# Optimization experiments

Measured on AMD Instinct MI355X. Metric: run time of the kernel, lower is better.

The kernel has to match this reference:

```python
import jax, jax.numpy as jnp
import numpy as np
from jax import lax

N_INPUT, N_HIDDEN, N_OUTPUT = 1024, 2048, 1024
T, B = 512, 64

def setup_inputs() -> dict:
    key = jax.random.key(0)
    k_x, k_ih, k_hh, k_out = jax.random.split(key, 4)
    stdv = 1.0 / np.sqrt(N_HIDDEN)
    xs = jax.random.normal(k_x, (T, B, N_INPUT), dtype=jnp.float32)
    # torch nn.Linear weights are [out_features, in_features], init U(-stdv, stdv)
    W_ih = jax.random.uniform(k_ih, (N_HIDDEN, N_INPUT), jnp.float32, -stdv, stdv)
    W_hh = jax.random.uniform(k_hh, (N_HIDDEN, N_HIDDEN), jnp.float32, -stdv, stdv)
    W_out = jax.random.uniform(k_out, (N_OUTPUT, N_HIDDEN), jnp.float32, -stdv, stdv)
    return {"xs": xs, "W_ih": W_ih, "W_hh": W_hh, "W_out": W_out}

def reference(xs, W_ih, W_hh, W_out):
    # xs: [T, B, n_input] time-major. state starts as None -> relu(W_ih x),
    # which equals relu(W_ih x + W_hh * 0), so h0 = zeros is exact.
    n_hidden = W_hh.shape[0]
    h0 = jnp.zeros((xs.shape[1], n_hidden), dtype=xs.dtype)

    def step(h, x):
        h = jax.nn.relu(x @ W_ih.T + h @ W_hh.T)  # [B, n_hidden]
        return h, h

    _, h_seq = lax.scan(step, h0, xs)        # [T, B, n_hidden]
    ys = h_seq @ W_out.T                     # [T, B, n_output]
    return jnp.transpose(ys, (1, 0, 2))      # [B, T, n_output] (transpose(0,1))
```

## Files before the change

### kernel.cpp

```cpp
#include <hip/hip_runtime.h>
#include <hip/hip_bf16.h>
#include <stdint.h>


#define TT 512
#define BB 64
#define NIN 1024
#define NH 2048
#define NOUT 1024

typedef __attribute__((ext_vector_type(8))) short bf8;
typedef __attribute__((ext_vector_type(4))) float f4;
typedef __attribute__((ext_vector_type(4))) unsigned int u4;

static __device__ __forceinline__ unsigned short f2bf(float f) {
  __hip_bfloat16 h = __float2bfloat16(f);
  return __builtin_bit_cast(unsigned short, h);
}
static __device__ __forceinline__ float bf2f(unsigned short v) {
  return __bfloat162float(__builtin_bit_cast(__hip_bfloat16, v));
}
static __device__ __forceinline__ u4 pack8(const float* f) {
  u4 r;
#pragma unroll
  for (int i = 0; i < 4; ++i) {
    unsigned lo = f2bf(f[2 * i]);
    unsigned hi = f2bf(f[2 * i + 1]);
    r[i] = lo | (hi << 16);
  }
  return r;
}

static __device__ __forceinline__ size_t sl_idx(int m, int col) {
  return ((((size_t)(m >> 6) * 4 + ((m & 63) >> 4)) * 64 + (col >> 5)) << 9) +
         (size_t)((m & 63) & 15) * 32 + (col & 31);
}

template <bool ABF, bool TRANS>
__global__ void gemm_bt(const void* __restrict__ Av, const float* __restrict__ Bw,
                        void* __restrict__ Cv, unsigned char* __restrict__ plane,
                        int M, int N, int K) {
  constexpr int BM = 128, BN = 128, BK = 32;
  __shared__ u4 As[BM * 4];
  __shared__ u4 Bs[BN * 4];
  const int nt = N / BN;
  const int mi = (int)blockIdx.x / nt;
  const int ni = (int)blockIdx.x % nt;
  const int m0 = mi * BM, n0 = ni * BN;
  const int t = threadIdx.x;
  const int l = t & 63, w = t >> 6, wr = w >> 1, wc = w & 1;
  const int lr = l & 15, lq = l >> 4;

  f4 acc[4][4] = {};

  const int srow = t >> 1;
  const int sc0 = (t & 1) * 2;
  const u4 msk = {0x7fff7fffu, 0x7fff7fffu, 0x7fff7fffu, 0x7fff7fffu};

  for (int kt = 0; kt < K; kt += BK) {
    if (ABF) {
      const unsigned short* A = (const unsigned short*)Av;
#pragma unroll
      for (int cc = 0; cc < 2; ++cc) {
        int c = sc0 + cc;
        u4 v = *(const u4*)(A + sl_idx(m0 + srow, kt + c * 8));
        v &= msk;
        As[srow * 4 + (c ^ ((srow ^ (srow >> 2)) & 3))] = v;
      }
    } else {
      const float* A = (const float*)Av;
#pragma unroll
      for (int cc = 0; cc < 2; ++cc) {
        int c = sc0 + cc;
        const float* p = A + (size_t)(m0 + srow) * K + kt + c * 8;
        float4 v0 = *(const float4*)p;
        float4 v1 = *(const float4*)(p + 4);
        float f[8] = {v0.x, v0.y, v0.z, v0.w, v1.x, v1.y, v1.z, v1.w};
        As[srow * 4 + (c ^ ((srow ^ (srow >> 2)) & 3))] = pack8(f);
      }
    }
#pragma unroll
    for (int cc = 0; cc < 2; ++cc) {
      int c = sc0 + cc;
      const float* p = Bw + (size_t)(n0 + srow) * K + kt + c * 8;
      float4 v0 = *(const float4*)p;
      float4 v1 = *(const float4*)(p + 4);
      float f[8] = {v0.x, v0.y, v0.z, v0.w, v1.x, v1.y, v1.z, v1.w};
      Bs[srow * 4 + (c ^ ((srow ^ (srow >> 2)) & 3))] = pack8(f);
    }
    __syncthreads();

    bf8 a[4], b[4];
#pragma unroll
    for (int i = 0; i < 4; ++i) {
      int ra = wr * 64 + i * 16 + lr;
      a[i] = __builtin_bit_cast(bf8, As[ra * 4 + (lq ^ ((ra ^ (ra >> 2)) & 3))]);
      int rb = wc * 64 + i * 16 + lr;
      b[i] = __builtin_bit_cast(bf8, Bs[rb * 4 + (lq ^ ((rb ^ (rb >> 2)) & 3))]);
    }
#pragma unroll
    for (int i = 0; i < 4; ++i)
#pragma unroll
      for (int j = 0; j < 4; ++j)
        acc[i][j] = __builtin_amdgcn_mfma_f32_16x16x32_bf16(a[i], b[j], acc[i][j], 0, 0, 0);
    __syncthreads();
  }

  if (TRANS) {
    float* C = (float*)Cv;
#pragma unroll
    for (int i = 0; i < 4; ++i)
#pragma unroll
      for (int j = 0; j < 4; ++j)
#pragma unroll
        for (int r = 0; r < 4; ++r) {
          int m = m0 + wr * 64 + i * 16 + lq * 4 + r;
          int n = n0 + wc * 64 + j * 16 + lr;
          C[(size_t)(m & 63) * (TT * NOUT) + (size_t)(m >> 6) * NOUT + n] = acc[i][j][r];
        }
  } else {
    unsigned short* C = (unsigned short*)Cv;
#pragma unroll
    for (int i = 0; i < 4; ++i)
#pragma unroll
      for (int j = 0; j < 4; ++j)
#pragma unroll
        for (int r = 0; r < 4; ++r) {
          int m = m0 + wr * 64 + i * 16 + lq * 4 + r;
          int n = n0 + wc * 64 + j * 16 + lr;
          unsigned short v = f2bf(acc[i][j][r]);
          size_t sl = sl_idx(m, n);
          C[sl] = (unsigned short)(v & 0x7fffu);
          unsigned long long bal = __ballot((v & 0x8000u) != 0);
          if ((l & 7) == 0)
            plane[sl >> 3] = (unsigned char)((bal >> (l & ~7)) & 0xffull);
        }
  }
}

__global__ __launch_bounds__(512, 2) void rnn_recur(unsigned short* __restrict__ hseq,
                                                    const unsigned char* __restrict__ plane,
                                                    const float* __restrict__ Whh,
                                                    unsigned* __restrict__ flags) {
  __shared__ u4 Wl[32 * 256];
  __shared__ float red[2][4][16][36];
  const int t = threadIdx.x;
  const int bid = (int)blockIdx.x;
  const int g = (bid & 7) >> 1;
  const int jb = ((bid >> 3) << 1) | (bid & 1);
  const int j0 = jb * 32;

  {
    const int jl = t >> 4;
    const int ci = t & 15;
#pragma unroll
    for (int q = 0; q < 16; ++q) {
      int cc = ci * 16 + q;
      const float* p = Whh + (size_t)(j0 + jl) * NH + cc * 8;
      float4 v0 = *(const float4*)p;
      float4 v1 = *(const float4*)(p + 4);
      float f[8] = {v0.x, v0.y, v0.z, v0.w, v1.x, v1.y, v1.z, v1.w};
      Wl[jl * 256 + (cc ^ (jl & 7))] = pack8(f);
    }
  }

  const int l = t & 63, w = t >> 6;
  const int lr = l & 15, lq = l >> 4;
  const int kg = w >> 1, jh = w & 1;

  char* hb = (char*)hseq;
  const size_t gofs = (size_t)g << 16;
  const u4 msk = {0x7fff7fffu, 0x7fff7fffu, 0x7fff7fffu, 0x7fff7fffu};

  const int wr_r = l >> 2;
  const int wjq = l & 3;
  const size_t wbyte = (size_t)wr_r * 64 + jh * 32 + wjq * 8;

  unsigned long long pre = 0;
  unsigned nib = 0;

  __syncthreads();

  if (w < 2) {
    size_t e0 = gofs + ((size_t)jb << 10) + wbyte;
    unsigned long long p0 = __hip_atomic_load((const unsigned long long*)(hb + e0),
                                              __ATOMIC_RELAXED, __HIP_MEMORY_SCOPE_AGENT);
    unsigned nib0 = (plane[e0 >> 4] >> (((e0 >> 3) & 1) * 4)) & 0xfu;
    unsigned long long hv = 0x8000800080008000ull;
#pragma unroll
    for (int i = 0; i < 4; ++i)
      if (!((nib0 >> i) & 1u)) hv |= ((p0 >> (16 * i)) & 0x7fffull) << (16 * i);
    __hip_atomic_store((unsigned long long*)(hb + e0), hv, __ATOMIC_RELAXED,
                       __HIP_MEMORY_SCOPE_AGENT);
    if (l == 0)
      __hip_atomic_store(flags + ((g * 64 + jb) * 2 + w), 1u, __ATOMIC_RELAXED,
                         __HIP_MEMORY_SCOPE_AGENT);
    size_t e1 = ((size_t)4 << 16) + gofs + ((size_t)jb << 10) + wbyte;
    pre = __hip_atomic_load((const unsigned long long*)(hb + e1), __ATOMIC_RELAXED,
                            __HIP_MEMORY_SCOPE_AGENT);
    nib = (plane[e1 >> 4] >> (((e1 >> 3) & 1) * 4)) & 0xfu;
  }

  for (int ts = 1; ts < TT; ++ts) {
    {
      const unsigned* fp = flags + ((g * 64 + kg * 16 + (l >> 1)) * 2 + (l & 1));
      long spins = 0;
      for (;;) {
        unsigned fv = (l < 32) ? __hip_atomic_load(fp, __ATOMIC_RELAXED,
                                                   __HIP_MEMORY_SCOPE_AGENT)
                               : 0xffffffffu;
        if (__ballot(fv >= (unsigned)ts) == ~0ull) break;
        __builtin_amdgcn_s_sleep(1);
        if (++spins > (1L << 22)) break;
      }
    }
    asm volatile("" ::: "memory");

    const size_t rowoff = (size_t)(l & 15) * 64 + (size_t)(l >> 4) * 16;
    const size_t base =
        (((size_t)(ts - 1) * 4) << 16) + gofs + ((size_t)(kg * 16) << 10) + rowoff;
    unsigned long long a0 = (unsigned long long)(uintptr_t)(hb + base);
    unsigned long long a1 = a0 + 4096;
    unsigned long long a2 = a0 + 8192;
    unsigned long long a3 = a0 + 12288;
    u4 av[16];
    int att = 0;
    for (;;) {
      asm volatile(
          "global_load_dwordx4 %0, %16, off sc0 sc1\n\t"
          "global_load_dwordx4 %1, %16, off offset:1024 sc0 sc1\n\t"
          "global_load_dwordx4 %2, %16, off offset:2048 sc0 sc1\n\t"
          "global_load_dwordx4 %3, %16, off offset:3072 sc0 sc1\n\t"
          "global_load_dwordx4 %4, %17, off sc0 sc1\n\t"
          "global_load_dwordx4 %5, %17, off offset:1024 sc0 sc1\n\t"
          "global_load_dwordx4 %6, %17, off offset:2048 sc0 sc1\n\t"
          "global_load_dwordx4 %7, %17, off offset:3072 sc0 sc1\n\t"
          "global_load_dwordx4 %8, %18, off sc0 sc1\n\t"
          "global_load_dwordx4 %9, %18, off offset:1024 sc0 sc1\n\t"
          "global_load_dwordx4 %10, %18, off offset:2048 sc0 sc1\n\t"
          "global_load_dwordx4 %11, %18, off offset:3072 sc0 sc1\n\t"
          "global_load_dwordx4 %12, %19, off sc0 sc1\n\t"
          "global_load_dwordx4 %13, %19, off offset:1024 sc0 sc1\n\t"
          "global_load_dwordx4 %14, %19, off offset:2048 sc0 sc1\n\t"
          "global_load_dwordx4 %15, %19, off offset:3072 sc0 sc1\n\t"
          "s_waitcnt vmcnt(0)"
          : "=&v"(av[0]), "=&v"(av[1]), "=&v"(av[2]), "=&v"(av[3]),
            "=&v"(av[4]), "=&v"(av[5]), "=&v"(av[6]), "=&v"(av[7]),
            "=&v"(av[8]), "=&v"(av[9]), "=&v"(av[10]), "=&v"(av[11]),
            "=&v"(av[12]), "=&v"(av[13]), "=&v"(av[14]), "=&v"(av[15])
          : "v"(a0), "v"(a1), "v"(a2), "v"(a3)
          : "memory");
      unsigned am = 0xffffffffu;
#pragma unroll
      for (int c = 0; c < 16; ++c)
#pragma unroll
        for (int d = 0; d < 4; ++d) am &= av[c][d];
      bool ok = (am & 0x80008000u) == 0x80008000u;
      if (__ballot(ok) == ~0ull) break;
      __builtin_amdgcn_s_sleep(1);
      if (++att > (1 << 20)) break;
    }

    f4 acc0 = {}, acc1 = {};
#pragma unroll
    for (int c = 0; c < 16; ++c) {
      u4 v = av[c] & msk;
      bf8 af = __builtin_bit_cast(bf8, v);
      int ci = kg * 64 + c * 4 + lq;
      bf8 bfr = __builtin_bit_cast(bf8, Wl[(jh * 16 + lr) * 256 + (ci ^ (lr & 7))]);
      if (c & 1)
        acc1 = __builtin_amdgcn_mfma_f32_16x16x32_bf16(af, bfr, acc1, 0, 0, 0);
      else
        acc0 = __builtin_amdgcn_mfma_f32_16x16x32_bf16(af, bfr, acc0, 0, 0, 0);
    }
    f4 a2v = acc0 + acc1;

    const int buf = ts & 1;
#pragma unroll
    for (int i = 0; i < 4; ++i) red[buf][kg][(l >> 4) * 4 + i][jh * 16 + (l & 15)] = a2v[i];
    __syncthreads();

    if (w < 2) {
      __builtin_amdgcn_s_setprio(1);
      float pf[4];
#pragma unroll
      for (int i = 0; i < 4; ++i) {
        unsigned pv = (unsigned)((pre >> (16 * i)) & 0xffffull);
        pv |= ((nib >> i) & 1u) << 15;
        pf[i] = bf2f((unsigned short)pv);
      }
      f4 s = {};
#pragma unroll
      for (int q = 0; q < 4; ++q) s += *(const f4*)&red[buf][q][wr_r][jh * 16 + wjq * 4];
      unsigned long long hv = 0;
#pragma unroll
      for (int i = 0; i < 4; ++i) {
        float v = s[i] + pf[i];
        v = v > 0.f ? v : 0.f;
        hv |= (unsigned long long)(unsigned short)(f2bf(v) | 0x8000u) << (16 * i);
      }
      size_t eo = (((size_t)ts * 4) << 16) + gofs + ((size_t)jb << 10) + wbyte;
      __hip_atomic_store((unsigned long long*)(hb + eo), hv, __ATOMIC_RELAXED,
                         __HIP_MEMORY_SCOPE_AGENT);
      if (l == 0)
        __hip_atomic_store(flags + ((g * 64 + jb) * 2 + w), (unsigned)(ts + 1),
                           __ATOMIC_RELAXED, __HIP_MEMORY_SCOPE_AGENT);
      if (ts + 1 < TT) {
        size_t en = (((size_t)(ts + 1) * 4) << 16) + gofs + ((size_t)jb << 10) + wbyte;
        pre = __hip_atomic_load((const unsigned long long*)(hb + en), __ATOMIC_RELAXED,
                                __HIP_MEMORY_SCOPE_AGENT);
        nib = (plane[en >> 4] >> (((en >> 3) & 1) * 4)) & 0xfu;
      }
      __builtin_amdgcn_s_setprio(0);
    }
  }
}

__global__ void kinit(unsigned* f) { f[threadIdx.x] = 0u; }

extern "C" void kernel_launch(void* const* d_in, const int* in_sizes, int n_in,
                              void* d_out, int out_size, void* d_ws, size_t ws_size,
                              hipStream_t stream) {
  const float* xs = (const float*)d_in[0];
  const float* Wih = (const float*)d_in[1];
  const float* Whh = (const float*)d_in[2];
  const float* Wout = (const float*)d_in[3];

  unsigned short* hseq = (unsigned short*)d_ws;
  unsigned char* plane = (unsigned char*)d_ws + ((size_t)TT * BB * NH * 2);
  unsigned* flags = (unsigned*)(plane + ((size_t)TT * BB * NH / 8));

  kinit<<<1, 512, 0, stream>>>(flags);

  gemm_bt<false, false><<<(TT * BB / 128) * (NH / 128), 256, 0, stream>>>(
      (const void*)xs, Wih, (void*)hseq, plane, TT * BB, NH, NIN);

  rnn_recur<<<256, 512, 0, stream>>>(hseq, plane, Whh, flags);

  gemm_bt<true, true><<<(TT * BB / 128) * (NOUT / 128), 256, 0, stream>>>(
      (const void*)hseq, Wout, d_out, plane, TT * BB, NOUT, NH);
}
```

Baseline: 3.848 ms.

## Repartition recurrence into 8 batch groups with register-resident W_hh slices

The recurrent kernel now splits the batch into 8 groups of 8 rows and the hidden dimension into 32 blocks of 64 columns, in place of 4 groups of 16 rows and 64 blocks of 32 columns. Each wave keeps its W_hh slice in registers instead of LDS. Each step cooperatively loads the previous hidden state once per block into LDS, with one contiguous 64-byte load per thread, instead of each wave doing 16 strided polling loads. The hidden-state slab layout changes to 8-row by 64-column tiles to match, and the upstream GEMM is updated to read and write that layout. The aim is fewer global polling loads and fewer flags to wait on per step. In exchange there is an extra barrier per step, higher register pressure from the weights, and half of each MFMA's rows are unused because only 8 batch rows are valid.

```diff
diff --git a/kernel.cpp b/kernel.cpp
--- a/kernel.cpp
+++ b/kernel.cpp
@@ -31,9 +31,9 @@
   return r;
 }
 
-static __device__ __forceinline__ size_t sl_idx(int m, int col) {
-  return ((((size_t)(m >> 6) * 4 + ((m & 63) >> 4)) * 64 + (col >> 5)) << 9) +
-         (size_t)((m & 63) & 15) * 32 + (col & 31);
+static __device__ __forceinline__ size_t sl_idx8(int m, int col) {
+  return ((((size_t)(m >> 6) * 8 + ((m & 63) >> 3)) * 32 + (col >> 6)) << 9) +
+         (size_t)((m & 63) & 7) * 64 + (col & 63);
 }
 
 template <bool ABF, bool TRANS>
@@ -63,7 +63,7 @@
 #pragma unroll
       for (int cc = 0; cc < 2; ++cc) {
         int c = sc0 + cc;
-        u4 v = *(const u4*)(A + sl_idx(m0 + srow, kt + c * 8));
+        u4 v = *(const u4*)(A + sl_idx8(m0 + srow, kt + c * 8));
         v &= msk;
         As[srow * 4 + (c ^ ((srow ^ (srow >> 2)) & 3))] = v;
       }
@@ -129,7 +129,7 @@
           int m = m0 + wr * 64 + i * 16 + lq * 4 + r;
           int n = n0 + wc * 64 + j * 16 + lr;
           unsigned short v = f2bf(acc[i][j][r]);
-          size_t sl = sl_idx(m, n);
+          size_t sl = sl_idx8(m, n);
           C[sl] = (unsigned short)(v & 0x7fffu);
           unsigned long long bal = __ballot((v & 0x8000u) != 0);
           if ((l & 7) == 0)
@@ -142,47 +142,45 @@
                                                     const unsigned char* __restrict__ plane,
                                                     const float* __restrict__ Whh,
                                                     unsigned* __restrict__ flags) {
-  __shared__ u4 Wl[32 * 256];
-  __shared__ float red[2][4][16][36];
+  __shared__ u4 hs[8 * 256];
+  __shared__ float red[2][4][8][68];
   const int t = threadIdx.x;
   const int bid = (int)blockIdx.x;
-  const int g = (bid & 7) >> 1;
-  const int jb = ((bid >> 3) << 1) | (bid & 1);
-  const int j0 = jb * 32;
-
-  {
-    const int jl = t >> 4;
-    const int ci = t & 15;
-#pragma unroll
-    for (int q = 0; q < 16; ++q) {
-      int cc = ci * 16 + q;
-      const float* p = Whh + (size_t)(j0 + jl) * NH + cc * 8;
+  const int g = bid & 7;
+  const int jb = bid >> 3;
+  const int j0 = jb * 64;
+
+  const int l = t & 63, w = t >> 6;
+  const int lr = l & 15, lq = l >> 4;
+  const int kg = w >> 1, jh = w & 1;
+
+  u4 wreg[2][16];
+#pragma unroll
+  for (int jt = 0; jt < 2; ++jt) {
+    const float* p0 = Whh + (size_t)(j0 + jh * 32 + jt * 16 + lr) * NH + kg * 512 + lq * 8;
+#pragma unroll
+    for (int ks = 0; ks < 16; ++ks) {
+      const float* p = p0 + ks * 32;
       float4 v0 = *(const float4*)p;
       float4 v1 = *(const float4*)(p + 4);
       float f[8] = {v0.x, v0.y, v0.z, v0.w, v1.x, v1.y, v1.z, v1.w};
-      Wl[jl * 256 + (cc ^ (jl & 7))] = pack8(f);
-    }
-  }
-
-  const int l = t & 63, w = t >> 6;
-  const int lr = l & 15, lq = l >> 4;
-  const int kg = w >> 1, jh = w & 1;
+      wreg[jt][ks] = pack8(f);
+    }
+  }
 
   char* hb = (char*)hseq;
-  const size_t gofs = (size_t)g << 16;
   const u4 msk = {0x7fff7fffu, 0x7fff7fffu, 0x7fff7fffu, 0x7fff7fffu};
 
-  const int wr_r = l >> 2;
-  const int wjq = l & 3;
-  const size_t wbyte = (size_t)wr_r * 64 + jh * 32 + wjq * 8;
+  const size_t wbyte = (size_t)(l >> 3) * 128 + (size_t)jh * 64 + (size_t)(l & 7) * 8;
+  const int sr = (t & 15) >> 1;
+  const int scb = ((t >> 4) << 3) + (t & 1) * 4;
+  const int fidx = (g * 32 + (t >> 4)) * 2 + (t & 1);
 
   unsigned long long pre = 0;
   unsigned nib = 0;
 
-  __syncthreads();
-
   if (w < 2) {
-    size_t e0 = gofs + ((size_t)jb << 10) + wbyte;
+    size_t e0 = (((size_t)g * 32 + jb) << 10) + wbyte;
     unsigned long long p0 = __hip_atomic_load((const unsigned long long*)(hb + e0),
                                               __ATOMIC_RELAXED, __HIP_MEMORY_SCOPE_AGENT);
     unsigned nib0 = (plane[e0 >> 4] >> (((e0 >> 3) & 1) * 4)) & 0xfu;
@@ -193,9 +191,9 @@
     __hip_atomic_store((unsigned long long*)(hb + e0), hv, __ATOMIC_RELAXED,
                        __HIP_MEMORY_SCOPE_AGENT);
     if (l == 0)
-      __hip_atomic_store(flags + ((g * 64 + jb) * 2 + w), 1u, __ATOMIC_RELAXED,
+      __hip_atomic_store(flags + ((g * 32 + jb) * 2 + w), 1u, __ATOMIC_RELAXED,
                          __HIP_MEMORY_SCOPE_AGENT);
-    size_t e1 = ((size_t)4 << 16) + gofs + ((size_t)jb << 10) + wbyte;
+    size_t e1 = (((size_t)(1 * 8 + g) * 32 + jb) << 10) + wbyte;
     pre = __hip_atomic_load((const unsigned long long*)(hb + e1), __ATOMIC_RELAXED,
                             __HIP_MEMORY_SCOPE_AGENT);
     nib = (plane[e1 >> 4] >> (((e1 >> 3) & 1) * 4)) & 0xfu;
@@ -203,12 +201,10 @@
 
   for (int ts = 1; ts < TT; ++ts) {
     {
-      const unsigned* fp = flags + ((g * 64 + kg * 16 + (l >> 1)) * 2 + (l & 1));
+      const unsigned* fp = flags + fidx;
       long spins = 0;
       for (;;) {
-        unsigned fv = (l < 32) ? __hip_atomic_load(fp, __ATOMIC_RELAXED,
-                                                   __HIP_MEMORY_SCOPE_AGENT)
-                               : 0xffffffffu;
+        unsigned fv = __hip_atomic_load(fp, __ATOMIC_RELAXED, __HIP_MEMORY_SCOPE_AGENT);
         if (__ballot(fv >= (unsigned)ts) == ~0ull) break;
         __builtin_amdgcn_s_sleep(1);
         if (++spins > (1L << 22)) break;
@@ -216,68 +212,63 @@
     }
     asm volatile("" ::: "memory");
 
-    const size_t rowoff = (size_t)(l & 15) * 64 + (size_t)(l >> 4) * 16;
-    const size_t base =
-        (((size_t)(ts - 1) * 4) << 16) + gofs + ((size_t)(kg * 16) << 10) + rowoff;
-    unsigned long long a0 = (unsigned long long)(uintptr_t)(hb + base);
-    unsigned long long a1 = a0 + 4096;
-    unsigned long long a2 = a0 + 8192;
-    unsigned long long a3 = a0 + 12288;
-    u4 av[16];
-    int att = 0;
-    for (;;) {
-      asm volatile(
-          "global_load_dwordx4 %0, %16, off sc0 sc1\n\t"
-          "global_load_dwordx4 %1, %16, off offset:1024 sc0 sc1\n\t"
-          "global_load_dwordx4 %2, %16, off offset:2048 sc0 sc1\n\t"
-          "global_load_dwordx4 %3, %16, off offset:3072 sc0 sc1\n\t"
-          "global_load_dwordx4 %4, %17, off sc0 sc1\n\t"
-          "global_load_dwordx4 %5, %17, off offset:1024 sc0 sc1\n\t"
-          "global_load_dwordx4 %6, %17, off offset:2048 sc0 sc1\n\t"
-          "global_load_dwordx4 %7, %17, off offset:3072 sc0 sc1\n\t"
-          "global_load_dwordx4 %8, %18, off sc0 sc1\n\t"
-          "global_load_dwordx4 %9, %18, off offset:1024 sc0 sc1\n\t"
-          "global_load_dwordx4 %10, %18, off offset:2048 sc0 sc1\n\t"
-          "global_load_dwordx4 %11, %18, off offset:3072 sc0 sc1\n\t"
-          "global_load_dwordx4 %12, %19, off sc0 sc1\n\t"
-          "global_load_dwordx4 %13, %19, off offset:1024 sc0 sc1\n\t"
-          "global_load_dwordx4 %14, %19, off offset:2048 sc0 sc1\n\t"
-          "global_load_dwordx4 %15, %19, off offset:3072 sc0 sc1\n\t"
-          "s_waitcnt vmcnt(0)"
-          : "=&v"(av[0]), "=&v"(av[1]), "=&v"(av[2]), "=&v"(av[3]),
-            "=&v"(av[4]), "=&v"(av[5]), "=&v"(av[6]), "=&v"(av[7]),
-            "=&v"(av[8]), "=&v"(av[9]), "=&v"(av[10]), "=&v"(av[11]),
-            "=&v"(av[12]), "=&v"(av[13]), "=&v"(av[14]), "=&v"(av[15])
-          : "v"(a0), "v"(a1), "v"(a2), "v"(a3)
-          : "memory");
-      unsigned am = 0xffffffffu;
-#pragma unroll
-      for (int c = 0; c < 16; ++c)
-#pragma unroll
-        for (int d = 0; d < 4; ++d) am &= av[c][d];
-      bool ok = (am & 0x80008000u) == 0x80008000u;
-      if (__ballot(ok) == ~0ull) break;
-      __builtin_amdgcn_s_sleep(1);
-      if (++att > (1 << 20)) break;
-    }
-
-    f4 acc0 = {}, acc1 = {};
-#pragma unroll
-    for (int c = 0; c < 16; ++c) {
-      u4 v = av[c] & msk;
-      bf8 af = __builtin_bit_cast(bf8, v);
-      int ci = kg * 64 + c * 4 + lq;
-      bf8 bfr = __builtin_bit_cast(bf8, Wl[(jh * 16 + lr) * 256 + (ci ^ (lr & 7))]);
-      if (c & 1)
-        acc1 = __builtin_amdgcn_mfma_f32_16x16x32_bf16(af, bfr, acc1, 0, 0, 0);
-      else
-        acc0 = __builtin_amdgcn_mfma_f32_16x16x32_bf16(af, bfr, acc0, 0, 0, 0);
-    }
-    f4 a2v = acc0 + acc1;
+    const size_t goff = ((((size_t)(ts - 1) * 8 + g) * 32) << 10) + (size_t)t * 64;
+    unsigned long long ga = (unsigned long long)(uintptr_t)(hb + goff);
+    u4 av[4];
+    {
+      long att = 0;
+      for (;;) {
+        asm volatile(
+            "global_load_dwordx4 %0, %4, off sc0 sc1\n\t"
+            "global_load_dwordx4 %1, %4, off offset:16 sc0 sc1\n\t"
+            "global_load_dwordx4 %2, %4, off offset:32 sc0 sc1\n\t"
+            "global_load_dwordx4 %3, %4, off offset:48 sc0 sc1\n\t"
+            "s_waitcnt vmcnt(0)"
+            : "=&v"(av[0]), "=&v"(av[1]), "=&v"(av[2]), "=&v"(av[3])
+            : "v"(ga)
+            : "memory");
+        unsigned am = 0xffffffffu;
+#pragma unroll
+        for (int c = 0; c < 4; ++c)
+#pragma unroll
+          for (int d = 0; d < 4; ++d) am &= av[c][d];
+        bool ok = (am & 0x80008000u) == 0x80008000u;
+        if (__ballot(ok) == ~0ull) break;
+        __builtin_amdgcn_s_sleep(1);
+        if (++att > (1L << 20)) break;
+      }
+    }
+#pragma unroll
+    for (int ch = 0; ch < 4; ++ch)
+      hs[sr * 256 + ((scb + ch) ^ sr)] = av[ch] & msk;
+    __syncthreads();
+
+    const int arow = l & 7;
+    f4 aA0 = {}, aA1 = {}, aB0 = {}, aB1 = {};
+#pragma unroll
+    for (int ks = 0; ks < 16; ++ks) {
+      u4 a = hs[arow * 256 + ((kg * 64 + ks * 4 + lq) ^ arow)];
+      bf8 af = __builtin_bit_cast(bf8, a);
+      bf8 b0 = __builtin_bit_cast(bf8, wreg[0][ks]);
+      bf8 b1 = __builtin_bit_cast(bf8, wreg[1][ks]);
+      if (ks & 1) {
+        aA1 = __builtin_amdgcn_mfma_f32_16x16x32_bf16(af, b0, aA1, 0, 0, 0);
+        aB1 = __builtin_amdgcn_mfma_f32_16x16x32_bf16(af, b1, aB1, 0, 0, 0);
+      } else {
+        aA0 = __builtin_amdgcn_mfma_f32_16x16x32_bf16(af, b0, aA0, 0, 0, 0);
+        aB0 = __builtin_amdgcn_mfma_f32_16x16x32_bf16(af, b1, aB0, 0, 0, 0);
+      }
+    }
+    f4 aA = aA0 + aA1, aB = aB0 + aB1;
 
     const int buf = ts & 1;
-#pragma unroll
-    for (int i = 0; i < 4; ++i) red[buf][kg][(l >> 4) * 4 + i][jh * 16 + (l & 15)] = a2v[i];
+    if (lq < 2) {
+#pragma unroll
+      for (int i = 0; i < 4; ++i) {
+        red[buf][kg][lq * 4 + i][jh * 32 + lr] = aA[i];
+        red[buf][kg][lq * 4 + i][jh * 32 + 16 + lr] = aB[i];
+      }
+    }
     __syncthreads();
 
     if (w < 2) {
@@ -289,9 +280,11 @@
         pv |= ((nib >> i) & 1u) << 15;
         pf[i] = bf2f((unsigned short)pv);
       }
+      const int rr = l >> 3;
+      const int jq = l & 7;
       f4 s = {};
 #pragma unroll
-      for (int q = 0; q < 4; ++q) s += *(const f4*)&red[buf][q][wr_r][jh * 16 + wjq * 4];
+      for (int q = 0; q < 4; ++q) s += *(const f4*)&red[buf][q][rr][jh * 32 + jq * 4];
       unsigned long long hv = 0;
 #pragma unroll
       for (int i = 0; i < 4; ++i) {
@@ -299,14 +292,14 @@
         v = v > 0.f ? v : 0.f;
         hv |= (unsigned long long)(unsigned short)(f2bf(v) | 0x8000u) << (16 * i);
       }
-      size_t eo = (((size_t)ts * 4) << 16) + gofs + ((size_t)jb << 10) + wbyte;
+      size_t eo = (((size_t)ts * 8 + g) * 32 + jb) * 1024 + wbyte;
       __hip_atomic_store((unsigned long long*)(hb + eo), hv, __ATOMIC_RELAXED,
                          __HIP_MEMORY_SCOPE_AGENT);
       if (l == 0)
-        __hip_atomic_store(flags + ((g * 64 + jb) * 2 + w), (unsigned)(ts + 1),
+        __hip_atomic_store(flags + ((g * 32 + jb) * 2 + w), (unsigned)(ts + 1),
                            __ATOMIC_RELAXED, __HIP_MEMORY_SCOPE_AGENT);
       if (ts + 1 < TT) {
-        size_t en = (((size_t)(ts + 1) * 4) << 16) + gofs + ((size_t)jb << 10) + wbyte;
+        size_t en = (((size_t)(ts + 1) * 8 + g) * 32 + jb) * 1024 + wbyte;
         pre = __hip_atomic_load((const unsigned long long*)(hb + en), __ATOMIC_RELAXED,
                                 __HIP_MEMORY_SCOPE_AGENT);
         nib = (plane[en >> 4] >> (((en >> 3) & 1) * 4)) & 0xfu;
```

Result: slower. 5.024 ms (+30.6%).

## Overlap hidden-state loads with MFMA via staged waitcnt and per-chunk readiness retry

Applied to the files above, without the earlier changes.

The recurrent step used to issue all 16 hidden-state loads, wait for every one, check readiness flags across the whole tile, and retry the whole set if any chunk was stale. Now the loads complete in four groups using partial vmcnt waits, and each 16-byte chunk gets its own readiness check and its MFMA as soon as that group arrives. Only chunks that fail the check are reloaded individually afterwards. The aim is to overlap memory latency with matrix math and avoid reloading the full tile on a partial miss. In exchange it adds per-chunk ballots and branches and relies on inline-asm waitcnt ordering being correct.

```diff
diff --git a/kernel.cpp b/kernel.cpp
--- a/kernel.cpp
+++ b/kernel.cpp
@@ -224,54 +224,95 @@
     unsigned long long a2 = a0 + 8192;
     unsigned long long a3 = a0 + 12288;
     u4 av[16];
-    int att = 0;
-    for (;;) {
-      asm volatile(
-          "global_load_dwordx4 %0, %16, off sc0 sc1\n\t"
-          "global_load_dwordx4 %1, %16, off offset:1024 sc0 sc1\n\t"
-          "global_load_dwordx4 %2, %16, off offset:2048 sc0 sc1\n\t"
-          "global_load_dwordx4 %3, %16, off offset:3072 sc0 sc1\n\t"
-          "global_load_dwordx4 %4, %17, off sc0 sc1\n\t"
-          "global_load_dwordx4 %5, %17, off offset:1024 sc0 sc1\n\t"
-          "global_load_dwordx4 %6, %17, off offset:2048 sc0 sc1\n\t"
-          "global_load_dwordx4 %7, %17, off offset:3072 sc0 sc1\n\t"
-          "global_load_dwordx4 %8, %18, off sc0 sc1\n\t"
-          "global_load_dwordx4 %9, %18, off offset:1024 sc0 sc1\n\t"
-          "global_load_dwordx4 %10, %18, off offset:2048 sc0 sc1\n\t"
-          "global_load_dwordx4 %11, %18, off offset:3072 sc0 sc1\n\t"
-          "global_load_dwordx4 %12, %19, off sc0 sc1\n\t"
-          "global_load_dwordx4 %13, %19, off offset:1024 sc0 sc1\n\t"
-          "global_load_dwordx4 %14, %19, off offset:2048 sc0 sc1\n\t"
-          "global_load_dwordx4 %15, %19, off offset:3072 sc0 sc1\n\t"
-          "s_waitcnt vmcnt(0)"
-          : "=&v"(av[0]), "=&v"(av[1]), "=&v"(av[2]), "=&v"(av[3]),
-            "=&v"(av[4]), "=&v"(av[5]), "=&v"(av[6]), "=&v"(av[7]),
-            "=&v"(av[8]), "=&v"(av[9]), "=&v"(av[10]), "=&v"(av[11]),
-            "=&v"(av[12]), "=&v"(av[13]), "=&v"(av[14]), "=&v"(av[15])
-          : "v"(a0), "v"(a1), "v"(a2), "v"(a3)
-          : "memory");
-      unsigned am = 0xffffffffu;
-#pragma unroll
-      for (int c = 0; c < 16; ++c)
-#pragma unroll
-        for (int d = 0; d < 4; ++d) am &= av[c][d];
-      bool ok = (am & 0x80008000u) == 0x80008000u;
-      if (__ballot(ok) == ~0ull) break;
-      __builtin_amdgcn_s_sleep(1);
-      if (++att > (1 << 20)) break;
-    }
+    asm volatile(
+        "global_load_dwordx4 %0, %16, off sc0 sc1\n\t"
+        "global_load_dwordx4 %1, %16, off offset:1024 sc0 sc1\n\t"
+        "global_load_dwordx4 %2, %16, off offset:2048 sc0 sc1\n\t"
+        "global_load_dwordx4 %3, %16, off offset:3072 sc0 sc1\n\t"
+        "global_load_dwordx4 %4, %17, off sc0 sc1\n\t"
+        "global_load_dwordx4 %5, %17, off offset:1024 sc0 sc1\n\t"
+        "global_load_dwordx4 %6, %17, off offset:2048 sc0 sc1\n\t"
+        "global_load_dwordx4 %7, %17, off offset:3072 sc0 sc1\n\t"
+        "global_load_dwordx4 %8, %18, off sc0 sc1\n\t"
+        "global_load_dwordx4 %9, %18, off offset:1024 sc0 sc1\n\t"
+        "global_load_dwordx4 %10, %18, off offset:2048 sc0 sc1\n\t"
+        "global_load_dwordx4 %11, %18, off offset:3072 sc0 sc1\n\t"
+        "global_load_dwordx4 %12, %19, off sc0 sc1\n\t"
+        "global_load_dwordx4 %13, %19, off offset:1024 sc0 sc1\n\t"
+        "global_load_dwordx4 %14, %19, off offset:2048 sc0 sc1\n\t"
+        "global_load_dwordx4 %15, %19, off offset:3072 sc0 sc1"
+        : "=&v"(av[0]), "=&v"(av[1]), "=&v"(av[2]), "=&v"(av[3]),
+          "=&v"(av[4]), "=&v"(av[5]), "=&v"(av[6]), "=&v"(av[7]),
+          "=&v"(av[8]), "=&v"(av[9]), "=&v"(av[10]), "=&v"(av[11]),
+          "=&v"(av[12]), "=&v"(av[13]), "=&v"(av[14]), "=&v"(av[15])
+        : "v"(a0), "v"(a1), "v"(a2), "v"(a3)
+        : "memory");
 
     f4 acc0 = {}, acc1 = {};
-#pragma unroll
-    for (int c = 0; c < 16; ++c) {
-      u4 v = av[c] & msk;
-      bf8 af = __builtin_bit_cast(bf8, v);
-      int ci = kg * 64 + c * 4 + lq;
-      bf8 bfr = __builtin_bit_cast(bf8, Wl[(jh * 16 + lr) * 256 + (ci ^ (lr & 7))]);
-      if (c & 1)
-        acc1 = __builtin_amdgcn_mfma_f32_16x16x32_bf16(af, bfr, acc1, 0, 0, 0);
-      else
-        acc0 = __builtin_amdgcn_mfma_f32_16x16x32_bf16(af, bfr, acc0, 0, 0, 0);
+    unsigned stale = 0;
+
+#define CHK(c)                                                                        \
+  {                                                                                   \
+    unsigned am_ = av[c][0] & av[c][1] & av[c][2] & av[c][3];                         \
+    if (__ballot((am_ & 0x80008000u) == 0x80008000u) == ~0ull) {                      \
+      u4 v_ = av[c] & msk;                                                            \
+      bf8 af_ = __builtin_bit_cast(bf8, v_);                                          \
+      int ci_ = kg * 64 + (c) * 4 + lq;                                               \
+      bf8 bf_ = __builtin_bit_cast(bf8, Wl[(jh * 16 + lr) * 256 + (ci_ ^ (lr & 7))]); \
+      if ((c) & 1)                                                                    \
+        acc1 = __builtin_amdgcn_mfma_f32_16x16x32_bf16(af_, bf_, acc1, 0, 0, 0);      \
+      else                                                                            \
+        acc0 = __builtin_amdgcn_mfma_f32_16x16x32_bf16(af_, bf_, acc0, 0, 0, 0);      \
+    } else                                                                            \
+      stale |= 1u << (c);                                                             \
+  }
+
+    asm volatile("s_waitcnt vmcnt(12)"
+                 : "+v"(av[0]), "+v"(av[1]), "+v"(av[2]), "+v"(av[3]));
+    __builtin_amdgcn_sched_barrier(0);
+    CHK(0) CHK(1) CHK(2) CHK(3)
+    asm volatile("s_waitcnt vmcnt(8)"
+                 : "+v"(av[4]), "+v"(av[5]), "+v"(av[6]), "+v"(av[7]));
+    __builtin_amdgcn_sched_barrier(0);
+    CHK(4) CHK(5) CHK(6) CHK(7)
+    asm volatile("s_waitcnt vmcnt(4)"
+                 : "+v"(av[8]), "+v"(av[9]), "+v"(av[10]), "+v"(av[11]));
+    __builtin_amdgcn_sched_barrier(0);
+    CHK(8) CHK(9) CHK(10) CHK(11)
+    asm volatile("s_waitcnt vmcnt(0)"
+                 : "+v"(av[12]), "+v"(av[13]), "+v"(av[14]), "+v"(av[15]));
+    __builtin_amdgcn_sched_barrier(0);
+    CHK(12) CHK(13) CHK(14) CHK(15)
+#undef CHK
+
+    {
+      long att = 0;
+      while (stale) {
+        int c = __builtin_ctz(stale);
+        unsigned long long ad =
+            a0 + (unsigned long long)(c >> 2) * 4096ull + (unsigned long long)(c & 3) * 1024ull;
+        for (;;) {
+          asm volatile(
+              "global_load_dwordx4 %0, %1, off sc0 sc1\n\t"
+              "s_waitcnt vmcnt(0)"
+              : "=&v"(av[c])
+              : "v"(ad)
+              : "memory");
+          unsigned am_ = av[c][0] & av[c][1] & av[c][2] & av[c][3];
+          if (__ballot((am_ & 0x80008000u) == 0x80008000u) == ~0ull) break;
+          __builtin_amdgcn_s_sleep(1);
+          if (++att > (1L << 20)) break;
+        }
+        u4 v_ = av[c] & msk;
+        bf8 af_ = __builtin_bit_cast(bf8, v_);
+        int ci_ = kg * 64 + c * 4 + lq;
+        bf8 bf_ = __builtin_bit_cast(bf8, Wl[(jh * 16 + lr) * 256 + (ci_ ^ (lr & 7))]);
+        if (c & 1)
+          acc1 = __builtin_amdgcn_mfma_f32_16x16x32_bf16(af_, bf_, acc1, 0, 0, 0);
+        else
+          acc0 = __builtin_amdgcn_mfma_f32_16x16x32_bf16(af_, bf_, acc0, 0, 0, 0);
+        stale &= stale - 1;
+      }
     }
     f4 a2v = acc0 + acc1;
 
```

Measured after the change: 4.605 ms. 1.2x slower.
